# Kernel optimization log

Hardware: AMD Instinct MI355X
Metric: run time of the kernel (lower is better)

## Reference

```python
import jax, jax.numpy as jnp
import numpy as np

N_QUBITS = 8
N_CYCLES = 4
C = jnp.complex64


def _mat2(a, b, c, d):
    # stack scalars (or batched scalars) into (..., 2, 2) complex matrix
    r0 = jnp.stack([jnp.asarray(a) + 0j, jnp.asarray(b) + 0j], axis=-1)
    r1 = jnp.stack([jnp.asarray(c) + 0j, jnp.asarray(d) + 0j], axis=-1)
    return jnp.stack([r0, r1], axis=-2).astype(C)


def rx(t):
    c = jnp.cos(t / 2)
    s = jnp.sin(t / 2)
    return _mat2(c, -1j * s, -1j * s, c)


def ry(t):
    c = jnp.cos(t / 2)
    s = jnp.sin(t / 2)
    return _mat2(c, -s, s, c)


def rz(t):
    e = jnp.exp(-0.5j * t)
    z = jnp.zeros_like(e)
    return _mat2(e, z, z, jnp.conj(e))


def u3(p):
    th, ph, lm = p[0], p[1], p[2]
    c = jnp.cos(th / 2)
    s = jnp.sin(th / 2)
    return _mat2(c, -jnp.exp(1j * lm) * s, jnp.exp(1j * ph) * s, jnp.exp(1j * (ph + lm)) * c)


def apply_1q(psi, U, w):
    # psi: (B, 2,2,...,2); U: (2,2) or batched (B,2,2)
    s = jnp.moveaxis(psi, 1 + w, -1)
    if U.ndim == 3:
        s = jnp.einsum('b...a,bca->b...c', s, U)
    else:
        s = jnp.einsum('...a,ca->...c', s, U)
    return jnp.moveaxis(s, -1, 1 + w)


def apply_ctrl(psi, U, c, t):
    # controlled-U: apply U on target wire t when control wire c is |1>
    s = jnp.moveaxis(psi, (1 + c, 1 + t), (-2, -1))
    s0 = s[..., 0, :]
    s1 = jnp.einsum('...a,ca->...c', s[..., 1, :], U)
    s = jnp.stack([s0, s1], axis=-2)
    return jnp.moveaxis(s, (-2, -1), (1 + c, 1 + t))


def expz(psi, w):
    # <Z_w> = P(bit_w=0) - P(bit_w=1)
    p = jnp.moveaxis(jnp.abs(psi) ** 2, 1 + w, -1).reshape(psi.shape[0], -1, 2).sum(axis=1)
    return p[:, 0] - p[:, 1]


def init_state(theta, phi):
    # hardware-efficient ansatz: N_CYCLES x [RY(theta), RZ(phi) on every wire, CNOT ring]
    B = theta.shape[0]
    psi = jnp.zeros((B,) + (2,) * N_QUBITS, C).at[(slice(None),) + (0,) * N_QUBITS].set(1.0 + 0j)
    X = jnp.array([[0, 1], [1, 0]], dtype=C)
    Ry = ry(theta)  # (B,2,2)
    Rz = rz(phi)
    for _ in range(N_CYCLES):
        for w in range(N_QUBITS):
            psi = apply_1q(psi, Ry, w)
            psi = apply_1q(psi, Rz, w)
        for w in range(N_QUBITS):
            psi = apply_ctrl(psi, X, w, (w + 1) % N_QUBITS)
    return psi


PAIRS_A = [(0, 1), (2, 3), (4, 5), (6, 7), (1, 2), (3, 4), (5, 6)]
PAIRS_B = [(1, 3), (5, 7), (3, 5)]


def branch(psi, rot, angles, u3p):
    for i, (c, t) in enumerate(PAIRS_A):
        psi = apply_ctrl(psi, rot(angles[i]), c, t)
    for i, w in enumerate([1, 3, 5, 7]):
        psi = apply_1q(psi, u3(u3p[i]), w)
    for i, (c, t) in enumerate(PAIRS_B):
        psi = apply_ctrl(psi, rot(angles[7 + i]), c, t)
    for i, w in enumerate([3, 7]):
        psi = apply_1q(psi, u3(u3p[4 + i]), w)
    return jnp.stack([expz(psi, 3), expz(psi, 7)], axis=1)  # (B, 2)


def setup_inputs() -> dict:
    key = jax.random.key(0)
    ks = jax.random.split(key, 12)
    B = 8192
    return {
        'theta': jax.random.uniform(ks[0], (B,), dtype=jnp.float32),
        'phi': jax.random.uniform(ks[1], (B,), dtype=jnp.float32),
        'angles_x': jax.random.normal(ks[2], (10,), dtype=jnp.float32),
        'angles_y': jax.random.normal(ks[3], (10,), dtype=jnp.float32),
        'angles_z': jax.random.normal(ks[4], (10,), dtype=jnp.float32),
        'u3_x': jax.random.normal(ks[5], (6, 3), dtype=jnp.float32),
        'u3_y': jax.random.normal(ks[6], (6, 3), dtype=jnp.float32),
        'u3_z': jax.random.normal(ks[7], (6, 3), dtype=jnp.float32),
        'W1': jax.random.normal(ks[8], (12, 6), dtype=jnp.float32) * 0.3,
        'b1': jax.random.normal(ks[9], (12,), dtype=jnp.float32) * 0.1,
        'W2': jax.random.normal(ks[10], (1, 12), dtype=jnp.float32) * 0.3,
        'b2': jax.random.normal(ks[11], (1,), dtype=jnp.float32) * 0.1,
    }


def reference(theta, phi, angles_x, angles_y, angles_z, u3_x, u3_y, u3_z, W1, b1, W2, b2):
    psi0 = init_state(theta, phi)
    x = branch(psi0, rx, angles_x, u3_x)  # CRX feature map
    y = branch(psi0, ry, angles_y, u3_y)  # CRY feature map
    z = branch(psi0, rz, angles_z, u3_z)  # CRZ feature map
    feats = jnp.concatenate([x, y, z], axis=1)  # (B, 6)
    h = jnp.tanh(feats @ W1.T + b1)
    return jax.nn.sigmoid(h @ W2.T + b2)  # (B, 1)
```

## Files before the change

### kernel.cpp

```cpp
#include <hip/hip_runtime.h>


struct cplx { float re, im; };
struct Gate { cplx u00, u01, u10, u11; };

struct M8 { unsigned r[8]; };

constexpr M8 midentity() {
    M8 F{};
    for (int i = 0; i < 8; ++i) F.r[i] = 1u << i;
    return F;
}

constexpr M8 ring_update(M8 F) {
    const int pc[8] = {7, 6, 5, 4, 3, 2, 1, 0};
    const int pt[8] = {6, 5, 4, 3, 2, 1, 0, 7};
    for (int g = 0; g < 8; ++g) F.r[pt[g]] ^= F.r[pc[g]];
    return F;
}

constexpr M8 minv(M8 F) {
    unsigned a[8] = {}, b[8] = {};
    for (int i = 0; i < 8; ++i) { a[i] = F.r[i]; b[i] = 1u << i; }
    for (int c = 0; c < 8; ++c) {
        int p = c;
        while (((a[p] >> c) & 1u) == 0u) ++p;
        unsigned ta = a[p]; a[p] = a[c]; a[c] = ta;
        unsigned tb = b[p]; b[p] = b[c]; b[c] = tb;
        for (int rr = 0; rr < 8; ++rr)
            if (rr != c && ((a[rr] >> c) & 1u)) { a[rr] ^= a[c]; b[rr] ^= b[c]; }
    }
    M8 R{};
    for (int i = 0; i < 8; ++i) R.r[i] = b[i];
    return R;
}

constexpr unsigned mcol(M8 F, int p) {
    unsigned m = 0;
    for (int q = 0; q < 8; ++q) m |= ((F.r[q] >> p) & 1u) << q;
    return m;
}

constexpr M8 F1 = ring_update(midentity());
constexpr M8 F2 = ring_update(F1);
constexpr M8 F3 = ring_update(F2);
constexpr M8 F4 = ring_update(F3);
constexpr M8 F1i = minv(F1);
constexpr M8 F2i = minv(F2);
constexpr M8 F3i = minv(F3);
constexpr M8 F4i = minv(F4);

__device__ __forceinline__ float shflx(float v, int m) { return __shfl_xor(v, m, 64); }

__device__ __forceinline__ cplx cfma2(cplx u, cplx a, cplx v, cplx b) {
    cplx r;
    r.re = u.re * a.re - u.im * a.im + v.re * b.re - v.im * b.im;
    r.im = u.re * a.im + u.im * a.re + v.re * b.im + v.im * b.re;
    return r;
}

template <unsigned X>
__device__ __forceinline__ void partner(const cplx a[4], cplx o[4]) {
    constexpr unsigned kx = X & 3u, lx = X >> 2;
    #pragma unroll
    for (int k = 0; k < 4; ++k) {
        const int ks = k ^ (int)kx;
        if constexpr (lx != 0) {
            o[k].re = shflx(a[ks].re, (int)lx);
            o[k].im = shflx(a[ks].im, (int)lx);
        } else {
            o[k] = a[ks];
        }
    }
}

template <unsigned X, unsigned R>
__device__ __forceinline__ void gate_ry(cplx a[4], float c, float s, int lane) {
    cplx o[4];
    partner<X>(a, o);
    const bool hl = (__popc(lane & (int)(R >> 2)) & 1) != 0;
    const float v = hl ? s : -s;
    #pragma unroll
    for (int k = 0; k < 4; ++k) {
        const int kp = __builtin_popcount((unsigned)k & (R & 3u)) & 1;
        const float sg = kp ? -v : v;
        a[k].re = c * a[k].re + sg * o[k].re;
        a[k].im = c * a[k].im + sg * o[k].im;
    }
}

template <unsigned X, unsigned R>
__device__ __forceinline__ void gate_u3(cplx a[4], const Gate& g, int lane) {
    cplx o[4];
    partner<X>(a, o);
    const bool hl = (__popc(lane & (int)(R >> 2)) & 1) != 0;
    cplx ca0, cb0, ca1, cb1;
    ca0.re = hl ? g.u11.re : g.u00.re;  ca0.im = hl ? g.u11.im : g.u00.im;
    cb0.re = hl ? g.u10.re : g.u01.re;  cb0.im = hl ? g.u10.im : g.u01.im;
    ca1.re = hl ? g.u00.re : g.u11.re;  ca1.im = hl ? g.u00.im : g.u11.im;
    cb1.re = hl ? g.u01.re : g.u10.re;  cb1.im = hl ? g.u01.im : g.u10.im;
    #pragma unroll
    for (int k = 0; k < 4; ++k) {
        const int kp = __builtin_popcount((unsigned)k & (R & 3u)) & 1;
        const cplx ca = kp ? ca1 : ca0;
        const cplx cb = kp ? cb1 : cb0;
        a[k] = cfma2(ca, a[k], cb, o[k]);
    }
}

template <unsigned X, unsigned RC>
__device__ __forceinline__ void gate_crx(cplx a[4], float c, float s, int lane) {
    cplx o[4];
    partner<X>(a, o);
    const bool cl = (__popc(lane & (int)(RC >> 2)) & 1) != 0;
    const float ce0 = cl ? c : 1.f, se0 = cl ? s : 0.f;
    const float ce1 = cl ? 1.f : c, se1 = cl ? 0.f : s;
    #pragma unroll
    for (int k = 0; k < 4; ++k) {
        const int kp = __builtin_popcount((unsigned)k & (RC & 3u)) & 1;
        const float ce = kp ? ce1 : ce0, se = kp ? se1 : se0;
        cplx n;
        n.re = ce * a[k].re + se * o[k].im;
        n.im = ce * a[k].im - se * o[k].re;
        a[k] = n;
    }
}

template <unsigned X, unsigned R, unsigned RC>
__device__ __forceinline__ void gate_cry(cplx a[4], float c, float s, int lane) {
    cplx o[4];
    partner<X>(a, o);
    const bool cl = (__popc(lane & (int)(RC >> 2)) & 1) != 0;
    const bool hl = (__popc(lane & (int)(R >> 2)) & 1) != 0;
    #pragma unroll
    for (int k = 0; k < 4; ++k) {
        const bool ctrl = cl ^ ((__builtin_popcount((unsigned)k & (RC & 3u)) & 1) != 0);
        const bool hi   = hl ^ ((__builtin_popcount((unsigned)k & (R & 3u)) & 1) != 0);
        const float ce = ctrl ? c : 1.f;
        const float sg = hi ? s : -s;
        const float se = ctrl ? sg : 0.f;
        cplx n;
        n.re = ce * a[k].re + se * o[k].re;
        n.im = ce * a[k].im + se * o[k].im;
        a[k] = n;
    }
}

template <unsigned R, unsigned RC>
__device__ __forceinline__ void gate_crz(cplx a[4], float c, float s, int lane) {
    const bool cl = (__popc(lane & (int)(RC >> 2)) & 1) != 0;
    const bool hl = (__popc(lane & (int)(R >> 2)) & 1) != 0;
    #pragma unroll
    for (int k = 0; k < 4; ++k) {
        const bool ctrl = cl ^ ((__builtin_popcount((unsigned)k & (RC & 3u)) & 1) != 0);
        const bool hi   = hl ^ ((__builtin_popcount((unsigned)k & (R & 3u)) & 1) != 0);
        const float fr = ctrl ? c : 1.f;
        const float sg = hi ? s : -s;
        const float fi = ctrl ? sg : 0.f;
        cplx n;
        n.re = fr * a[k].re - fi * a[k].im;
        n.im = fr * a[k].im + fi * a[k].re;
        a[k] = n;
    }
}

template <int C>
__device__ __forceinline__ void cycle_ry(cplx a[4], float c, float s, int lane) {
    constexpr M8 F  = (C == 1) ? F1 : (C == 2) ? F2 : F3;
    constexpr M8 Fi = (C == 1) ? F1i : (C == 2) ? F2i : F3i;
    gate_ry<mcol(Fi, 7), F.r[7]>(a, c, s, lane);
    gate_ry<mcol(Fi, 6), F.r[6]>(a, c, s, lane);
    gate_ry<mcol(Fi, 5), F.r[5]>(a, c, s, lane);
    gate_ry<mcol(Fi, 4), F.r[4]>(a, c, s, lane);
    gate_ry<mcol(Fi, 3), F.r[3]>(a, c, s, lane);
    gate_ry<mcol(Fi, 2), F.r[2]>(a, c, s, lane);
    gate_ry<mcol(Fi, 1), F.r[1]>(a, c, s, lane);
    gate_ry<mcol(Fi, 0), F.r[0]>(a, c, s, lane);
}

template <int C>
__device__ __forceinline__ void cycle_diag(cplx a[4], float phw, int lane) {
    constexpr M8 F = (C == 1) ? F1 : (C == 2) ? F2 : F3;
    int hp[8];
    #pragma unroll
    for (int p = 0; p < 8; ++p) hp[p] = __popc(lane & (int)(F.r[p] >> 2)) & 1;
    #pragma unroll
    for (int k = 0; k < 4; ++k) {
        int n = 0;
        #pragma unroll
        for (int p = 0; p < 8; ++p) {
            const int kb = __builtin_popcount(F.r[p] & 3u & (unsigned)k) & 1;
            n += kb ? (1 - hp[p]) : hp[p];
        }
        float sn, cn;
        __sincosf(phw * (float)(n - 4), &sn, &cn);
        cplx v;
        v.re = cn * a[k].re - sn * a[k].im;
        v.im = cn * a[k].im + sn * a[k].re;
        a[k] = v;
    }
}

struct BranchG { float rc[10], rs[10]; Gate u[6]; };

template <int KIND, int PC, int PT>
__device__ __forceinline__ void crot(cplx a[4], float c, float s, int lane) {
    constexpr unsigned X = mcol(F4i, PT), R = F4.r[PT], RC = F4.r[PC];
    if constexpr (KIND == 0)      gate_crx<X, RC>(a, c, s, lane);
    else if constexpr (KIND == 1) gate_cry<X, R, RC>(a, c, s, lane);
    else                          gate_crz<R, RC>(a, c, s, lane);
}

template <int KIND>
__device__ __forceinline__ void run_branch(const BranchG& G, cplx a[4],
                                           int lane, float& o3, float& o7) {
    crot<KIND, 7, 6>(a, G.rc[0], G.rs[0], lane);
    crot<KIND, 5, 4>(a, G.rc[1], G.rs[1], lane);
    crot<KIND, 3, 2>(a, G.rc[2], G.rs[2], lane);
    crot<KIND, 1, 0>(a, G.rc[3], G.rs[3], lane);
    crot<KIND, 6, 5>(a, G.rc[4], G.rs[4], lane);
    crot<KIND, 4, 3>(a, G.rc[5], G.rs[5], lane);
    crot<KIND, 2, 1>(a, G.rc[6], G.rs[6], lane);
    gate_u3<mcol(F4i, 6), F4.r[6]>(a, G.u[0], lane);
    gate_u3<mcol(F4i, 4), F4.r[4]>(a, G.u[1], lane);
    gate_u3<mcol(F4i, 2), F4.r[2]>(a, G.u[2], lane);
    gate_u3<mcol(F4i, 0), F4.r[0]>(a, G.u[3], lane);
    crot<KIND, 6, 4>(a, G.rc[7], G.rs[7], lane);
    crot<KIND, 2, 0>(a, G.rc[8], G.rs[8], lane);
    crot<KIND, 4, 2>(a, G.rc[9], G.rs[9], lane);
    gate_u3<mcol(F4i, 4), F4.r[4]>(a, G.u[4], lane);
    gate_u3<mcol(F4i, 0), F4.r[0]>(a, G.u[5], lane);

    constexpr unsigned R3 = F4.r[4], R7 = F4.r[0];
    const bool h3 = (__popc(lane & (int)(R3 >> 2)) & 1) != 0;
    const bool h7 = (__popc(lane & (int)(R7 >> 2)) & 1) != 0;
    float p3 = 0.f, p7 = 0.f;
    #pragma unroll
    for (int k = 0; k < 4; ++k) {
        const float m = a[k].re * a[k].re + a[k].im * a[k].im;
        const bool s3 = h3 ^ ((__builtin_popcount((unsigned)k & (R3 & 3u)) & 1) != 0);
        const bool s7 = h7 ^ ((__builtin_popcount((unsigned)k & (R7 & 3u)) & 1) != 0);
        p3 += s3 ? -m : m;
        p7 += s7 ? -m : m;
    }
    #pragma unroll
    for (int off = 32; off >= 1; off >>= 1) {
        p3 += shflx(p3, off);
        p7 += shflx(p7, off);
    }
    o3 = p3;
    o7 = p7;
}

__global__ void __launch_bounds__(192, 8) qcnn_kernel(
    const float* __restrict__ theta, const float* __restrict__ phi,
    const float* __restrict__ ax, const float* __restrict__ ay, const float* __restrict__ az,
    const float* __restrict__ u3x, const float* __restrict__ u3y, const float* __restrict__ u3z,
    const float* __restrict__ W1, const float* __restrict__ b1,
    const float* __restrict__ W2, const float* __restrict__ b2,
    float* __restrict__ out, int B) {
    __shared__ BranchG gb[3];
    __shared__ __align__(16) float st[512];
    __shared__ float feats[6];

    const int t    = threadIdx.x;
    const int wv   = t >> 6;
    const int lane = t & 63;
    const int b    = blockIdx.x;

    if (wv == 1) {
        const int tt = lane;
        if (tt < 30) {
            const int br = tt / 10, i = tt - br * 10;
            const float* ang = (br == 0) ? ax : (br == 1) ? ay : az;
            float s, c;
            __sincosf(0.5f * ang[i], &s, &c);
            gb[br].rc[i] = c;
            gb[br].rs[i] = s;
        } else if (tt >= 32 && tt < 50) {
            const int idx = tt - 32, br = idx / 6, row = idx - br * 6;
            const float* up = (br == 0) ? u3x : (br == 1) ? u3y : u3z;
            const float th = up[row * 3 + 0], ph = up[row * 3 + 1], lm = up[row * 3 + 2];
            float sth, cth; __sincosf(0.5f * th, &sth, &cth);
            float sph, cph; __sincosf(ph, &sph, &cph);
            float slm, clm; __sincosf(lm, &slm, &clm);
            float spl, cpl; __sincosf(ph + lm, &spl, &cpl);
            Gate G;
            G.u00 = {cth, 0.f};
            G.u01 = {-clm * sth, -slm * sth};
            G.u10 = {cph * sth, sph * sth};
            G.u11 = {cpl * cth, spl * cth};
            gb[br].u[row] = G;
        }
    }

    if (wv == 0) {
        const float thv = theta[b], phv = phi[b];
        float s, c, sp, cp;
        __sincosf(0.5f * thv, &s, &c);
        __sincosf(0.5f * phv, &sp, &cp);

        cplx a[4];
        {
            float f = 1.f;
            #pragma unroll
            for (int bb = 0; bb < 6; ++bb) f *= ((lane >> bb) & 1) ? s : c;
            const int pl = __popc(lane);
            float e0s, e0c;
            __sincosf(phv * (float)(pl - 4), &e0s, &e0c);
            const float e1c = cp * cp - sp * sp;
            const float e1s = 2.f * sp * cp;
            cplx e0{e0c, e0s};
            cplx e1{e0.re * e1c - e0.im * e1s, e0.re * e1s + e0.im * e1c};
            cplx e2{e1.re * e1c - e1.im * e1s, e1.re * e1s + e1.im * e1c};
            const float cc = c * c, cs = c * s, ss = s * s;
            a[0] = {f * cc * e0.re, f * cc * e0.im};
            a[1] = {f * cs * e1.re, f * cs * e1.im};
            a[2] = {f * cs * e1.re, f * cs * e1.im};
            a[3] = {f * ss * e2.re, f * ss * e2.im};
        }

        cycle_ry<1>(a, c, s, lane);  cycle_diag<1>(a, phv, lane);
        cycle_ry<2>(a, c, s, lane);  cycle_diag<2>(a, phv, lane);
        cycle_ry<3>(a, c, s, lane);  cycle_diag<3>(a, phv, lane);

        float4* sv = (float4*)st;
        sv[lane * 2 + 0] = make_float4(a[0].re, a[0].im, a[1].re, a[1].im);
        sv[lane * 2 + 1] = make_float4(a[2].re, a[2].im, a[3].re, a[3].im);
    }
    __syncthreads();

    {
        cplx a[4];
        const float4* sv = (const float4*)st;
        const float4 v0 = sv[lane * 2 + 0], v1 = sv[lane * 2 + 1];
        a[0] = {v0.x, v0.y}; a[1] = {v0.z, v0.w};
        a[2] = {v1.x, v1.y}; a[3] = {v1.z, v1.w};

        float o3, o7;
        if (wv == 0)      run_branch<0>(gb[0], a, lane, o3, o7);
        else if (wv == 1) run_branch<1>(gb[1], a, lane, o3, o7);
        else              run_branch<2>(gb[2], a, lane, o3, o7);
        if (lane == 0) {
            feats[wv * 2 + 0] = o3;
            feats[wv * 2 + 1] = o7;
        }
    }
    __syncthreads();

    if (wv == 0) {
        float fv[6];
        #pragma unroll
        for (int i = 0; i < 6; ++i) fv[i] = feats[i];
        float val = 0.f;
        if (lane < 12) {
            float h = b1[lane];
            #pragma unroll
            for (int k = 0; k < 6; ++k) h = fmaf(W1[lane * 6 + k], fv[k], h);
            const float e = __expf(2.f * h);
            val = W2[lane] * ((e - 1.f) / (e + 1.f));
        }
        val += shflx(val, 1);
        val += shflx(val, 2);
        val += shflx(val, 4);
        val += shflx(val, 8);
        if (lane == 0) out[b] = 1.f / (1.f + __expf(-(val + b2[0])));
    }
}

extern "C" void kernel_launch(void* const* d_in, const int* in_sizes, int n_in,
                              void* d_out, int out_size, void* d_ws, size_t ws_size,
                              hipStream_t stream) {
    const float* theta = (const float*)d_in[0];
    const float* phi   = (const float*)d_in[1];
    const float* ax    = (const float*)d_in[2];
    const float* ay    = (const float*)d_in[3];
    const float* az    = (const float*)d_in[4];
    const float* u3x   = (const float*)d_in[5];
    const float* u3y   = (const float*)d_in[6];
    const float* u3z   = (const float*)d_in[7];
    const float* W1    = (const float*)d_in[8];
    const float* b1    = (const float*)d_in[9];
    const float* W2    = (const float*)d_in[10];
    const float* b2    = (const float*)d_in[11];
    const int B = in_sizes[0];

    qcnn_kernel<<<B, 192, 0, stream>>>(theta, phi, ax, ay, az,
                                       u3x, u3y, u3z, W1, b1, W2, b2,
                                       (float*)d_out, B);
}
```

Measured before the change: 131.6 us.

## Map one wavefront per sample, running all three branches sequentially in-register

Each 64-lane wavefront now handles one batch sample end to end, with four samples per 256-thread block. Previously each sample used three wavefronts that split the branches, with shared-memory handoff and two block barriers. The init state is computed once per wave and reused by the three branches in registers, which removes the LDS round trip, the feats exchange and the redundant per-sample block setup. In exchange there is less parallelism per sample and higher per-wave latency, and the gate setup is now amortized over four samples.

```diff
diff --git a/kernel.cpp b/kernel.cpp
--- a/kernel.cpp
+++ b/kernel.cpp
@@ -212,8 +212,12 @@
 }
 
 template <int KIND>
-__device__ __forceinline__ void run_branch(const BranchG& G, cplx a[4],
+__device__ __forceinline__ void run_branch(const BranchG& G, const cplx p0[4],
                                            int lane, float& o3, float& o7) {
+    cplx a[4];
+    #pragma unroll
+    for (int k = 0; k < 4; ++k) a[k] = p0[k];
+
     crot<KIND, 7, 6>(a, G.rc[0], G.rs[0], lane);
     crot<KIND, 5, 4>(a, G.rc[1], G.rs[1], lane);
     crot<KIND, 3, 2>(a, G.rc[2], G.rs[2], lane);
@@ -252,7 +256,7 @@
     o7 = p7;
 }
 
-__global__ void __launch_bounds__(192, 8) qcnn_kernel(
+__global__ void __launch_bounds__(256, 8) qcnn_kernel(
     const float* __restrict__ theta, const float* __restrict__ phi,
     const float* __restrict__ ax, const float* __restrict__ ay, const float* __restrict__ az,
     const float* __restrict__ u3x, const float* __restrict__ u3y, const float* __restrict__ u3z,
@@ -260,112 +264,90 @@
     const float* __restrict__ W2, const float* __restrict__ b2,
     float* __restrict__ out, int B) {
     __shared__ BranchG gb[3];
-    __shared__ __align__(16) float st[512];
-    __shared__ float feats[6];
 
     const int t    = threadIdx.x;
-    const int wv   = t >> 6;
     const int lane = t & 63;
-    const int b    = blockIdx.x;
-
-    if (wv == 1) {
-        const int tt = lane;
-        if (tt < 30) {
-            const int br = tt / 10, i = tt - br * 10;
-            const float* ang = (br == 0) ? ax : (br == 1) ? ay : az;
-            float s, c;
-            __sincosf(0.5f * ang[i], &s, &c);
-            gb[br].rc[i] = c;
-            gb[br].rs[i] = s;
-        } else if (tt >= 32 && tt < 50) {
-            const int idx = tt - 32, br = idx / 6, row = idx - br * 6;
-            const float* up = (br == 0) ? u3x : (br == 1) ? u3y : u3z;
-            const float th = up[row * 3 + 0], ph = up[row * 3 + 1], lm = up[row * 3 + 2];
-            float sth, cth; __sincosf(0.5f * th, &sth, &cth);
-            float sph, cph; __sincosf(ph, &sph, &cph);
-            float slm, clm; __sincosf(lm, &slm, &clm);
-            float spl, cpl; __sincosf(ph + lm, &spl, &cpl);
-            Gate G;
-            G.u00 = {cth, 0.f};
-            G.u01 = {-clm * sth, -slm * sth};
-            G.u10 = {cph * sth, sph * sth};
-            G.u11 = {cpl * cth, spl * cth};
-            gb[br].u[row] = G;
-        }
-    }
-
-    if (wv == 0) {
-        const float thv = theta[b], phv = phi[b];
-        float s, c, sp, cp;
-        __sincosf(0.5f * thv, &s, &c);
-        __sincosf(0.5f * phv, &sp, &cp);
-
-        cplx a[4];
-        {
-            float f = 1.f;
-            #pragma unroll
-            for (int bb = 0; bb < 6; ++bb) f *= ((lane >> bb) & 1) ? s : c;
-            const int pl = __popc(lane);
-            float e0s, e0c;
-            __sincosf(phv * (float)(pl - 4), &e0s, &e0c);
-            const float e1c = cp * cp - sp * sp;
-            const float e1s = 2.f * sp * cp;
-            cplx e0{e0c, e0s};
-            cplx e1{e0.re * e1c - e0.im * e1s, e0.re * e1s + e0.im * e1c};
-            cplx e2{e1.re * e1c - e1.im * e1s, e1.re * e1s + e1.im * e1c};
-            const float cc = c * c, cs = c * s, ss = s * s;
-            a[0] = {f * cc * e0.re, f * cc * e0.im};
-            a[1] = {f * cs * e1.re, f * cs * e1.im};
-            a[2] = {f * cs * e1.re, f * cs * e1.im};
-            a[3] = {f * ss * e2.re, f * ss * e2.im};
-        }
-
-        cycle_ry<1>(a, c, s, lane);  cycle_diag<1>(a, phv, lane);
-        cycle_ry<2>(a, c, s, lane);  cycle_diag<2>(a, phv, lane);
-        cycle_ry<3>(a, c, s, lane);  cycle_diag<3>(a, phv, lane);
-
-        float4* sv = (float4*)st;
-        sv[lane * 2 + 0] = make_float4(a[0].re, a[0].im, a[1].re, a[1].im);
-        sv[lane * 2 + 1] = make_float4(a[2].re, a[2].im, a[3].re, a[3].im);
+    const int b    = blockIdx.x * 4 + (t >> 6);
+
+    const float thv = (b < B) ? theta[b] : 0.f;
+    const float phv = (b < B) ? phi[b]   : 0.f;
+
+    if (t < 30) {
+        const int br = t / 10, i = t - br * 10;
+        const float* ang = (br == 0) ? ax : (br == 1) ? ay : az;
+        float s, c;
+        __sincosf(0.5f * ang[i], &s, &c);
+        gb[br].rc[i] = c;
+        gb[br].rs[i] = s;
+    } else if (t >= 32 && t < 50) {
+        const int idx = t - 32, br = idx / 6, row = idx - br * 6;
+        const float* up = (br == 0) ? u3x : (br == 1) ? u3y : u3z;
+        const float th = up[row * 3 + 0], ph = up[row * 3 + 1], lm = up[row * 3 + 2];
+        float sth, cth; __sincosf(0.5f * th, &sth, &cth);
+        float sph, cph; __sincosf(ph, &sph, &cph);
+        float slm, clm; __sincosf(lm, &slm, &clm);
+        float spl, cpl; __sincosf(ph + lm, &spl, &cpl);
+        Gate G;
+        G.u00 = {cth, 0.f};
+        G.u01 = {-clm * sth, -slm * sth};
+        G.u10 = {cph * sth, sph * sth};
+        G.u11 = {cpl * cth, spl * cth};
+        gb[br].u[row] = G;
     }
     __syncthreads();
-
+    if (b >= B) return;
+
+    float s, c, sp, cp;
+    __sincosf(0.5f * thv, &s, &c);
+    __sincosf(0.5f * phv, &sp, &cp);
+
+    cplx a[4];
     {
-        cplx a[4];
-        const float4* sv = (const float4*)st;
-        const float4 v0 = sv[lane * 2 + 0], v1 = sv[lane * 2 + 1];
-        a[0] = {v0.x, v0.y}; a[1] = {v0.z, v0.w};
-        a[2] = {v1.x, v1.y}; a[3] = {v1.z, v1.w};
-
-        float o3, o7;
-        if (wv == 0)      run_branch<0>(gb[0], a, lane, o3, o7);
-        else if (wv == 1) run_branch<1>(gb[1], a, lane, o3, o7);
-        else              run_branch<2>(gb[2], a, lane, o3, o7);
-        if (lane == 0) {
-            feats[wv * 2 + 0] = o3;
-            feats[wv * 2 + 1] = o7;
-        }
-    }
-    __syncthreads();
-
-    if (wv == 0) {
-        float fv[6];
+        float f = 1.f;
         #pragma unroll
-        for (int i = 0; i < 6; ++i) fv[i] = feats[i];
-        float val = 0.f;
-        if (lane < 12) {
-            float h = b1[lane];
-            #pragma unroll
-            for (int k = 0; k < 6; ++k) h = fmaf(W1[lane * 6 + k], fv[k], h);
-            const float e = __expf(2.f * h);
-            val = W2[lane] * ((e - 1.f) / (e + 1.f));
-        }
-        val += shflx(val, 1);
-        val += shflx(val, 2);
-        val += shflx(val, 4);
-        val += shflx(val, 8);
-        if (lane == 0) out[b] = 1.f / (1.f + __expf(-(val + b2[0])));
-    }
+        for (int bb = 0; bb < 6; ++bb) f *= ((lane >> bb) & 1) ? s : c;
+        const int pl = __popc(lane);
+        float e0s, e0c;
+        __sincosf(phv * (float)(pl - 4), &e0s, &e0c);
+        const float e1c = cp * cp - sp * sp;
+        const float e1s = 2.f * sp * cp;
+        cplx e0{e0c, e0s};
+        cplx e1{e0.re * e1c - e0.im * e1s, e0.re * e1s + e0.im * e1c};
+        cplx e2{e1.re * e1c - e1.im * e1s, e1.re * e1s + e1.im * e1c};
+        const float cc = c * c, cs = c * s, ss = s * s;
+        a[0] = {f * cc * e0.re, f * cc * e0.im};
+        a[1] = {f * cs * e1.re, f * cs * e1.im};
+        a[2] = {f * cs * e1.re, f * cs * e1.im};
+        a[3] = {f * ss * e2.re, f * ss * e2.im};
+    }
+
+    cycle_ry<1>(a, c, s, lane);  cycle_diag<1>(a, phv, lane);
+    cycle_ry<2>(a, c, s, lane);  cycle_diag<2>(a, phv, lane);
+    cycle_ry<3>(a, c, s, lane);  cycle_diag<3>(a, phv, lane);
+
+    float f0, f1, f2, f3, f4, f5;
+    run_branch<0>(gb[0], a, lane, f0, f1);
+    run_branch<1>(gb[1], a, lane, f2, f3);
+    run_branch<2>(gb[2], a, lane, f4, f5);
+
+    float val = 0.f;
+    if (lane < 12) {
+        float h = b1[lane];
+        const float* w = W1 + lane * 6;
+        h = fmaf(w[0], f0, h);
+        h = fmaf(w[1], f1, h);
+        h = fmaf(w[2], f2, h);
+        h = fmaf(w[3], f3, h);
+        h = fmaf(w[4], f4, h);
+        h = fmaf(w[5], f5, h);
+        const float e = __expf(2.f * h);
+        val = W2[lane] * ((e - 1.f) / (e + 1.f));
+    }
+    val += shflx(val, 1);
+    val += shflx(val, 2);
+    val += shflx(val, 4);
+    val += shflx(val, 8);
+    if (lane == 0) out[b] = 1.f / (1.f + __expf(-(val + b2[0])));
 }
 
 extern "C" void kernel_launch(void* const* d_in, const int* in_sizes, int n_in,
@@ -385,7 +367,8 @@
     const float* b2    = (const float*)d_in[11];
     const int B = in_sizes[0];
 
-    qcnn_kernel<<<B, 192, 0, stream>>>(theta, phi, ax, ay, az,
-                                       u3x, u3y, u3z, W1, b1, W2, b2,
-                                       (float*)d_out, B);
-}
+    const int blocks = (B + 3) / 4;
+    qcnn_kernel<<<blocks, 256, 0, stream>>>(theta, phi, ax, ay, az,
+                                            u3x, u3y, u3z, W1, b1, W2, b2,
+                                            (float*)d_out, B);
+}
```

Measured after the change: 128.7 us. 2.2% less time.
